# Optimization experiments

Measured on AMD Instinct MI355X. Metric: run time of the kernel, lower is better.

The kernel has to match this reference:

```python
import jax, jax.numpy as jnp
import numpy as np

B, T, C, H, L, E, K, V = 4, 1024, 1024, 16, 2, 8, 2, 32000
HD = C // H
CAP = B * T * K // E  # expert capacity with capacity_factor=1.0 -> 2048


def setup_inputs() -> dict:
    key = jax.random.key(0)
    ks = iter(jax.random.split(key, 16))
    def rn(shape, s=0.02):
        return jax.random.normal(next(ks), shape, jnp.float32) * s
    return {
        'input_ids': jax.random.randint(next(ks), (B, T), 0, V),
        'noise': jax.random.normal(next(ks), (L, B, T, E), jnp.float32),
        'tok_emb': rn((V, C)),
        'pos_emb': rn((T, C)),
        'ln1_w': jnp.ones((L, C)), 'ln1_b': jnp.zeros((L, C)),
        'qkv_w': rn((L, 3 * C, C)), 'out_w': rn((L, C, C)),
        'ln2_w': jnp.ones((L, C)), 'ln2_b': jnp.zeros((L, C)),
        'rt_w': rn((L, E, C)), 'rt_b': jnp.zeros((L, E)),
        'nz_w': rn((L, E, C)), 'nz_b': jnp.zeros((L, E)),
        'e_w1': rn((L, E, 4 * C, C)), 'e_b1': jnp.zeros((L, E, 4 * C)),
        'e_w2': rn((L, E, C, 4 * C)), 'e_b2': jnp.zeros((L, E, C)),
        'lnf_w': jnp.ones((C,)), 'lnf_b': jnp.zeros((C,)),
        'head_w': rn((1, C)), 'head_b': jnp.zeros((1,)),
    }


def _ln(x, w, b):
    m = jnp.mean(x, -1, keepdims=True)
    v = jnp.mean(jnp.square(x - m), -1, keepdims=True)
    return (x - m) * jax.lax.rsqrt(v + 1e-5) * w + b


def _attn(x, qkv_w, out_w):
    # non-causal flash-attention equivalent (softmax_scale = 1/sqrt(head_size))
    qkv = (x @ qkv_w.T).reshape(B, T, 3, H, HD)
    q, k, v = qkv[:, :, 0], qkv[:, :, 1], qkv[:, :, 2]
    s = jnp.einsum('bthd,bshd->bhts', q, k) / np.float32(np.sqrt(HD))
    p = jax.nn.softmax(s, axis=-1)
    o = jnp.einsum('bhts,bshd->bthd', p, v).reshape(B, T, C)
    return o @ out_w.T


def _moe(x, rt_w, rt_b, nz_w, nz_b, w1, b1, w2, b2, noise):
    logits = x @ rt_w.T + rt_b                      # [B,T,E]
    noise_logits = x @ nz_w.T + nz_b
    noisy = logits + noise * jax.nn.softplus(noise_logits)
    topv, topi = jax.lax.top_k(noisy, K)            # [B,T,K]
    gates = jax.nn.softmax(topv, axis=-1)           # softmax over sparse (-inf filled) logits == softmax over top-k
    oh = jax.nn.one_hot(topi, E, dtype=x.dtype)     # [B,T,K,E]
    router = jnp.einsum('btk,btke->bte', gates, oh)
    N = B * T
    flat_x = x.reshape(N, C)
    flat_r = router.reshape(N, E)
    flat_i = topi.reshape(N, K)
    updates = jnp.zeros_like(flat_x)
    for i in range(E):  # per-expert gather -> FFN -> scatter, capacity-limited in token order
        mask = jnp.any(flat_i == i, axis=-1)        # [N]
        pos = jnp.cumsum(mask) - 1
        keep = mask & (pos < CAP)
        sel = jnp.argsort(jnp.logical_not(keep))[:CAP]  # stable: kept tokens first, original order
        valid = keep[sel].astype(x.dtype)
        xi = flat_x[sel]                             # [CAP,C]
        h = jax.nn.relu(xi @ w1[i].T + b1[i])
        out = h @ w2[i].T + b2[i]
        gate = flat_r[sel, i] * valid
        updates = updates.at[sel].add(out * gate[:, None])
    return updates.reshape(B, T, C)


def reference(input_ids, noise, tok_emb, pos_emb, ln1_w, ln1_b, qkv_w, out_w,
              ln2_w, ln2_b, rt_w, rt_b, nz_w, nz_b, e_w1, e_b1, e_w2, e_b2,
              lnf_w, lnf_b, head_w, head_b):
    x = tok_emb[input_ids] + pos_emb[None, :T]
    for l in range(L):
        x = x + _attn(_ln(x, ln1_w[l], ln1_b[l]), qkv_w[l], out_w[l])
        x = x + _moe(_ln(x, ln2_w[l], ln2_b[l]), rt_w[l], rt_b[l], nz_w[l], nz_b[l],
                     e_w1[l], e_b1[l], e_w2[l], e_b2[l], noise[l])
    x = _ln(x, lnf_w, lnf_b)
    return jnp.mean(x, axis=1) @ head_w.T + head_b  # [B,1]
```

## Files before the change

kernel.cpp:

```cpp
#include <hip/hip_runtime.h>
#include <hip/hip_bf16.h>
#include <math.h>

namespace {

constexpr int B = 4, T = 1024, C = 1024, Hh = 16, L = 2, E = 8, HD = 64;
constexpr int NTOK = B * T;
constexpr int CAP = 1024;
constexpr int C3 = 3 * C, C4 = 4 * C;

typedef __attribute__((ext_vector_type(8))) short bf16x8;
typedef __attribute__((ext_vector_type(8))) short short8;
typedef __attribute__((ext_vector_type(4))) float f32x4;

static __device__ __forceinline__ short f2b(float f) {
  __hip_bfloat16 h = __float2bfloat16(f);
  return *reinterpret_cast<short*>(&h);
}
static __device__ __forceinline__ float b2f(unsigned short u) {
  union { unsigned int i; float f; } v; v.i = (unsigned int)u << 16; return v.f;
}

#define SWZ(row, kb) (((row) << 7) + ((kb) ^ (((row) & 7) << 4)))

static __device__ __forceinline__ void gload16(const void* g, void* l) {
  __builtin_amdgcn_global_load_lds((const __attribute__((address_space(1))) void*)g,
                                   (__attribute__((address_space(3))) void*)l, 16, 0, 0);
}

__global__ __launch_bounds__(256) void cvt4_kernel(
    const float* __restrict__ s0, const float* __restrict__ s1,
    const float* __restrict__ s2, const float* __restrict__ s3,
    unsigned short* __restrict__ d0, unsigned short* __restrict__ d1,
    unsigned short* __restrict__ d2, unsigned short* __restrict__ d3) {
  constexpr size_t N0 = (size_t)L * C3 * C, N1 = (size_t)L * C * C;
  constexpr size_t N2 = (size_t)L * E * C4 * C;
  size_t i = ((size_t)blockIdx.x * 256 + threadIdx.x) * 16;
  const float* s; unsigned short* d; size_t off;
  if (i < N0)                { s = s0; d = d0; off = i; }
  else if (i < N0 + N1)      { s = s1; d = d1; off = i - N0; }
  else if (i < N0 + N1 + N2) { s = s2; d = d2; off = i - N0 - N1; }
  else                       { s = s3; d = d3; off = i - N0 - N1 - N2; }
  float4 v0 = *(const float4*)(s + off);
  float4 v1 = *(const float4*)(s + off + 4);
  float4 v2 = *(const float4*)(s + off + 8);
  float4 v3 = *(const float4*)(s + off + 12);
  short8 r0, r1;
  r0[0] = f2b(v0.x); r0[1] = f2b(v0.y); r0[2] = f2b(v0.z); r0[3] = f2b(v0.w);
  r0[4] = f2b(v1.x); r0[5] = f2b(v1.y); r0[6] = f2b(v1.z); r0[7] = f2b(v1.w);
  r1[0] = f2b(v2.x); r1[1] = f2b(v2.y); r1[2] = f2b(v2.z); r1[3] = f2b(v2.w);
  r1[4] = f2b(v3.x); r1[5] = f2b(v3.y); r1[6] = f2b(v3.z); r1[7] = f2b(v3.w);
  *(short8*)(d + off) = r0;
  *(short8*)(d + off + 8) = r1;
}

__global__ __launch_bounds__(256) void embed_kernel(const int* __restrict__ ids,
    const float* __restrict__ tok, const float* __restrict__ pos, float* __restrict__ x) {
  int idx = blockIdx.x * 256 + threadIdx.x;
  int n = idx >> 8;
  int c4 = idx & 255;
  int t = n & (T - 1);
  int id = ids[n];
  float4 a = ((const float4*)(tok + (size_t)id * C))[c4];
  float4 p = ((const float4*)(pos + (size_t)t * C))[c4];
  float4 r{a.x + p.x, a.y + p.y, a.z + p.z, a.w + p.w};
  ((float4*)x)[idx] = r;
}

__global__ __launch_bounds__(256) void ln_kernel(const float* __restrict__ in,
    const unsigned short* __restrict__ eo, const int* __restrict__ slot0,
    const int* __restrict__ slot1, float* __restrict__ xupd,
    float* __restrict__ out, unsigned short* __restrict__ outb,
    const float* __restrict__ w, const float* __restrict__ b) {
  constexpr size_t SLICE = (size_t)E * CAP * C;
  __shared__ float red[8];
  int row = blockIdx.x, tid = threadIdx.x;
  float4 v = ((const float4*)(in + (size_t)row * C))[tid];
  if (eo) {
    int s0 = slot0[row], s1 = slot1[row];
    auto addslot = [&](int s) {
      if (s < 0) return;
      const unsigned short* p0 = eo + (size_t)s * C + tid * 4;
      short4 u = *(const short4*)p0;
      short4 u2 = *(const short4*)(p0 + SLICE);
      v.x += b2f((unsigned short)u.x) + b2f((unsigned short)u2.x);
      v.y += b2f((unsigned short)u.y) + b2f((unsigned short)u2.y);
      v.z += b2f((unsigned short)u.z) + b2f((unsigned short)u2.z);
      v.w += b2f((unsigned short)u.w) + b2f((unsigned short)u2.w);
    };
    addslot(s0);
    addslot(s1);
    if (xupd) ((float4*)(xupd + (size_t)row * C))[tid] = v;
  }
  float s = v.x + v.y + v.z + v.w;
  #pragma unroll
  for (int off = 32; off > 0; off >>= 1) s += __shfl_down(s, off);
  if ((tid & 63) == 0) red[tid >> 6] = s;
  __syncthreads();
  float mean = (red[0] + red[1] + red[2] + red[3]) * (1.f / C);
  __syncthreads();
  float dx = v.x - mean, dy = v.y - mean, dz = v.z - mean, dw = v.w - mean;
  float sq = dx * dx + dy * dy + dz * dz + dw * dw;
  #pragma unroll
  for (int off = 32; off > 0; off >>= 1) sq += __shfl_down(sq, off);
  if ((tid & 63) == 0) red[tid >> 6] = sq;
  __syncthreads();
  float var = (red[0] + red[1] + red[2] + red[3]) * (1.f / C);
  float rs = rsqrtf(var + 1e-5f);
  float4 wc = ((const float4*)w)[tid];
  float4 bc = ((const float4*)b)[tid];
  float4 o{dx * rs * wc.x + bc.x, dy * rs * wc.y + bc.y,
           dz * rs * wc.z + bc.z, dw * rs * wc.w + bc.w};
  if (out) ((float4*)(out + (size_t)row * C))[tid] = o;
  if (outb) {
    short4 ob{f2b(o.x), f2b(o.y), f2b(o.z), f2b(o.w)};
    *(short4*)(outb + (size_t)row * C + tid * 4) = ob;
  }
}

__global__ __launch_bounds__(256) void ln2_router_kernel(const float* __restrict__ in,
    unsigned short* __restrict__ outb,
    const float* __restrict__ w, const float* __restrict__ b,
    const float* __restrict__ rt_w, const float* __restrict__ rt_b,
    const float* __restrict__ nz_w, const float* __restrict__ nz_b,
    const float* __restrict__ noise,
    int* __restrict__ i0, int* __restrict__ i1, float* __restrict__ g0,
    float* __restrict__ g1, int* __restrict__ slot0, int* __restrict__ slot1)
{
  __shared__ float red[8];
  __shared__ float racc[4][16];
  int row = blockIdx.x, tid = threadIdx.x;
  float4 v = ((const float4*)(in + (size_t)row * C))[tid];
  float s = v.x + v.y + v.z + v.w;
  #pragma unroll
  for (int off = 32; off > 0; off >>= 1) s += __shfl_down(s, off);
  if ((tid & 63) == 0) red[tid >> 6] = s;
  __syncthreads();
  float mean = (red[0] + red[1] + red[2] + red[3]) * (1.f / C);
  __syncthreads();
  float dx = v.x - mean, dy = v.y - mean, dz = v.z - mean, dw = v.w - mean;
  float sq = dx * dx + dy * dy + dz * dz + dw * dw;
  #pragma unroll
  for (int off = 32; off > 0; off >>= 1) sq += __shfl_down(sq, off);
  if ((tid & 63) == 0) red[tid >> 6] = sq;
  __syncthreads();
  float var = (red[0] + red[1] + red[2] + red[3]) * (1.f / C);
  float rs = rsqrtf(var + 1e-5f);
  float4 wc = ((const float4*)w)[tid];
  float4 bc = ((const float4*)b)[tid];
  float4 o{dx * rs * wc.x + bc.x, dy * rs * wc.y + bc.y,
           dz * rs * wc.z + bc.z, dw * rs * wc.w + bc.w};
  short4 ob{f2b(o.x), f2b(o.y), f2b(o.z), f2b(o.w)};
  *(short4*)(outb + (size_t)row * C + tid * 4) = ob;

  float loc[16];
  #pragma unroll
  for (int e = 0; e < 8; e++) {
    float4 rw = *(const float4*)(rt_w + (size_t)e * C + tid * 4);
    float4 nw = *(const float4*)(nz_w + (size_t)e * C + tid * 4);
    loc[e]     = o.x * rw.x + o.y * rw.y + o.z * rw.z + o.w * rw.w;
    loc[8 + e] = o.x * nw.x + o.y * nw.y + o.z * nw.z + o.w * nw.w;
  }
  #pragma unroll
  for (int e = 0; e < 16; e++) {
    #pragma unroll
    for (int off = 32; off > 0; off >>= 1) loc[e] += __shfl_down(loc[e], off);
  }
  if ((tid & 63) == 0) {
    #pragma unroll
    for (int e = 0; e < 16; e++) racc[tid >> 6][e] = loc[e];
  }
  __syncthreads();
  if (tid == 0) {
    float nv[8];
    #pragma unroll
    for (int e = 0; e < 8; e++) {
      float lgt = racc[0][e] + racc[1][e] + racc[2][e] + racc[3][e] + rt_b[e];
      float nl = racc[0][8 + e] + racc[1][8 + e] + racc[2][8 + e] + racc[3][8 + e] + nz_b[e];
      float sp = fmaxf(nl, 0.f) + log1pf(expf(-fabsf(nl)));
      nv[e] = lgt + noise[(size_t)row * E + e] * sp;
    }
    float v0 = -INFINITY, v1 = -INFINITY; int b0 = -1, b1 = -1;
    #pragma unroll
    for (int e = 0; e < 8; e++) {
      float vv = nv[e];
      if (vv > v0)      { v1 = v0; b1 = b0; v0 = vv; b0 = e; }
      else if (vv > v1) { v1 = vv; b1 = e; }
    }
    float ex = expf(v1 - v0);
    float inv = 1.f / (1.f + ex);
    i0[row] = b0; i1[row] = b1;
    g0[row] = inv; g1[row] = ex * inv;
    slot0[row] = -1; slot1[row] = -1;
  }
}

template<bool GATHER, bool RELU, bool BIAS, bool XCDMAP, int OUTMODE, int SPLITK>
__global__ __launch_bounds__(512, 2) void gemm8p(
    const unsigned short* __restrict__ A, const unsigned short* __restrict__ W,
    const float* __restrict__ bias, unsigned short* __restrict__ Cout,
    const int* __restrict__ rowidx, const float* __restrict__ rowscale,
    const int* __restrict__ cnts, int M, int N, int Kd,
    size_t strideA, size_t strideW, size_t strideOut, int strideBias, int GY)
{
  __shared__ alignas(16) char smem[131072];
  int bx, by, e, ksl;
  if constexpr (XCDMAP) {
    int fid = blockIdx.x; e = fid & 7; int r1 = fid >> 3;
    ksl = r1 & (SPLITK - 1); int wi = r1 / SPLITK;
    by = wi % GY; bx = wi / GY;
  } else { bx = blockIdx.x; by = blockIdx.y; e = 0; ksl = 0; }
  int Mr = M;
  if (cnts) { int cc = cnts[e]; Mr = cc < M ? cc : M; }
  int row0 = by * 256, col0 = bx * 256;
  if (row0 >= Mr) return;

  const int kLen = Kd / SPLITK;
  const unsigned short* Ap = A + (size_t)e * strideA;
  const unsigned short* Wp = W + (size_t)e * strideW;
  const int* ridx = rowidx ? rowidx + (size_t)e * CAP : nullptr;

  int t = threadIdx.x;
  int l = t & 63, lm = l & 15, lg = l >> 4;
  int w = t >> 6, wm = w >> 2, wn = w & 3;

  const char* srcA[2];
  const char* srcB[2];
  #pragma unroll
  for (int j = 0; j < 2; j++) {
    int flat = t + j * 512;
    int row = flat >> 2;
    int c16 = (flat & 3) ^ ((row >> 1) & 3);
    int ga;
    if constexpr (GATHER) {
      int ar = row0 + row; if (ar >= Mr) ar = Mr - 1; ga = ridx[ar];
    } else ga = row0 + row;
    srcA[j] = (const char*)Ap + (size_t)ga * Kd * 2 + (size_t)ksl * kLen * 2 + c16 * 16;
    srcB[j] = (const char*)Wp + (size_t)(col0 + row) * Kd * 2 + (size_t)ksl * kLen * 2 + c16 * 16;
  }
  int dst0 = t * 16, dst1 = t * 16 + 8192;

  auto STAGE = [&](int buf, int op, int kh, int kt) {
    size_t goff = (size_t)kt * 128 + kh * 64;
    char* base = smem + buf * 65536 + op * 32768 + kh * 16384;
    if (op) {
      gload16(srcB[0] + goff, base + dst0);
      gload16(srcB[1] + goff, base + dst1);
    } else {
      gload16(srcA[0] + goff, base + dst0);
      gload16(srcA[1] + goff, base + dst1);
    }
  };

  int colswz = (lg ^ ((lm >> 1) & 3)) * 16;

  f32x4 acc[8][4];
  #pragma unroll
  for (int i = 0; i < 8; i++)
    #pragma unroll
    for (int j = 0; j < 4; j++) acc[i][j] = f32x4{0.f, 0.f, 0.f, 0.f};

  STAGE(0, 0, 0, 0); STAGE(0, 1, 0, 0); STAGE(0, 0, 1, 0); STAGE(0, 1, 1, 0);
  asm volatile("s_waitcnt vmcnt(0)" ::: "memory");
  __builtin_amdgcn_s_barrier();

  int NT = kLen >> 6;
  bf16x8 bfr[4];
  for (int k = 0; k < NT; k++) {
    int cur = k & 1, nxt = cur ^ 1;
    bool pf = (k + 1 < NT);
    #pragma unroll
    for (int ph = 0; ph < 4; ph++) {
      const int ks = ph >> 1, mh = ph & 1;
      bf16x8 afr[4];
      #pragma unroll
      for (int i = 0; i < 4; i++) {
        int row = wm * 128 + (mh * 4 + i) * 16 + lm;
        afr[i] = *(const bf16x8*)(smem + cur * 65536 + ks * 16384 + row * 64 + colswz);
      }
      if (mh == 0) {
        #pragma unroll
        for (int i = 0; i < 4; i++) {
          int row = wn * 64 + i * 16 + lm;
          bfr[i] = *(const bf16x8*)(smem + cur * 65536 + 32768 + ks * 16384 + row * 64 + colswz);
        }
      }
      if (pf) STAGE(nxt, mh, ks, k + 1);
      if (mh == 1) {
        if (pf) asm volatile("s_waitcnt vmcnt(4)" ::: "memory");
        else    asm volatile("s_waitcnt vmcnt(0)" ::: "memory");
      }
      __builtin_amdgcn_s_barrier();
      __builtin_amdgcn_s_setprio(1);
      #pragma unroll
      for (int i = 0; i < 4; i++)
        #pragma unroll
        for (int ni = 0; ni < 4; ni++)
          acc[mh * 4 + i][ni] =
              __builtin_amdgcn_mfma_f32_16x16x32_bf16(afr[i], bfr[ni], acc[mh * 4 + i][ni], 0, 0, 0);
      __builtin_amdgcn_s_setprio(0);
      __builtin_amdgcn_s_barrier();
    }
  }

  float cbias[4];
  #pragma unroll
  for (int ni = 0; ni < 4; ni++)
    cbias[ni] = (BIAS && ksl == 0) ? bias[(size_t)e * strideBias + col0 + wn * 64 + ni * 16 + lm] : 0.f;

  #pragma unroll
  for (int mi = 0; mi < 8; mi++) {
    #pragma unroll
    for (int rr = 0; rr < 4; rr++) {
      int m = row0 + wm * 128 + mi * 16 + lg * 4 + rr;
      if (m >= Mr) continue;
      if constexpr (OUTMODE == 0) {
        unsigned short* cp = Cout + (size_t)e * strideOut + (size_t)m * N + col0 + wn * 64 + lm;
        #pragma unroll
        for (int ni = 0; ni < 4; ni++) {
          float v = acc[mi][ni][rr] + cbias[ni];
          if constexpr (RELU) v = fmaxf(v, 0.f);
          cp[ni * 16] = (unsigned short)f2b(v);
        }
      } else {
        float sc = rowscale[(size_t)e * CAP + m];
        unsigned short* cp = Cout + (size_t)ksl * ((size_t)E * CAP * N)
                             + ((size_t)e * CAP + m) * N + col0 + wn * 64 + lm;
        #pragma unroll
        for (int ni = 0; ni < 4; ni++) {
          float v = acc[mi][ni][rr] + cbias[ni];
          cp[ni * 16] = (unsigned short)f2b(sc * v);
        }
      }
    }
  }
}

__global__ __launch_bounds__(256) void gemm_proj(
    const unsigned short* __restrict__ A, const unsigned short* __restrict__ W,
    float* __restrict__ Cout, int M, int N, int Kd)
{
  int bx = blockIdx.x, by = blockIdx.y;
  int row0 = by * 128, col0 = bx * 128;

  __shared__ alignas(16) char smem[32768];
  char* Ab = smem;
  char* Bb = smem + 16384;

  int t = threadIdx.x, w = t >> 6, l = t & 63;
  int lm = l & 15, lg = l >> 4;
  int wr = w >> 1, wc = w & 1;

  int lrow8 = l >> 3;
  int scol = ((l & 7) ^ lrow8) << 4;
  const char* srcA[4];
  const char* srcB[4];
  #pragma unroll
  for (int i = 0; i < 4; i++) {
    int seg = w * 4 + i;
    int rloc = seg * 8 + lrow8;
    srcA[i] = (const char*)A + (size_t)(row0 + rloc) * Kd * 2 + scol;
    srcB[i] = (const char*)W + (size_t)(col0 + rloc) * Kd * 2 + scol;
  }

  f32x4 acc[4][4];
  #pragma unroll
  for (int i = 0; i < 4; i++)
    #pragma unroll
    for (int j = 0; j < 4; j++) acc[i][j] = f32x4{0.f, 0.f, 0.f, 0.f};

  int NT = Kd >> 6;
  for (int kt = 0; kt < NT; kt++) {
    __syncthreads();
    #pragma unroll
    for (int i = 0; i < 4; i++) {
      int seg = w * 4 + i;
      gload16(srcA[i], Ab + seg * 1024);
      gload16(srcB[i], Bb + seg * 1024);
      srcA[i] += 128;
      srcB[i] += 128;
    }
    __syncthreads();
    #pragma unroll
    for (int ks = 0; ks < 2; ks++) {
      bf16x8 af[4], bfr[4];
      #pragma unroll
      for (int mi = 0; mi < 4; mi++)
        af[mi] = *(const bf16x8*)(Ab + SWZ(wr * 64 + mi * 16 + lm, ks * 64 + lg * 16));
      #pragma unroll
      for (int ni = 0; ni < 4; ni++)
        bfr[ni] = *(const bf16x8*)(Bb + SWZ(wc * 64 + ni * 16 + lm, ks * 64 + lg * 16));
      #pragma unroll
      for (int mi = 0; mi < 4; mi++)
        #pragma unroll
        for (int ni = 0; ni < 4; ni++)
          acc[mi][ni] = __builtin_amdgcn_mfma_f32_16x16x32_bf16(af[mi], bfr[ni], acc[mi][ni], 0, 0, 0);
    }
  }

  #pragma unroll
  for (int mi = 0; mi < 4; mi++) {
    #pragma unroll
    for (int rr = 0; rr < 4; rr++) {
      int m = row0 + wr * 64 + mi * 16 + lg * 4 + rr;
      float* cp = Cout + (size_t)m * N + col0 + wc * 64 + lm;
      #pragma unroll
      for (int ni = 0; ni < 4; ni++) cp[ni * 16] += acc[mi][ni][rr];
    }
  }
}

__global__ __launch_bounds__(256) void attn_mfma(const unsigned short* __restrict__ qkv,
                                                 unsigned short* __restrict__ ao) {
  __shared__ alignas(16) char smem[20480];
  char* Ks = smem;
  char* Vt = smem + 4096;
  char* Pb = smem + 12288;

  int t = threadIdx.x, w = t >> 6, lane = t & 63, lm = lane & 15, lg = lane >> 4;
  int qt = blockIdx.x, bh = blockIdx.y, b = bh >> 4, h = bh & 15;
  const unsigned short* base = qkv + (size_t)b * T * C3;

  bf16x8 qf[2];
  {
    int qrow = qt * 64 + w * 16 + lm;
    const unsigned short* qp = base + (size_t)qrow * C3 + h * HD + lg * 8;
    qf[0] = *(const bf16x8*)qp;
    qf[1] = *(const bf16x8*)(qp + 32);
  }

  f32x4 o[4];
  #pragma unroll
  for (int i = 0; i < 4; i++) o[i] = f32x4{0.f, 0.f, 0.f, 0.f};
  float mrun[4] = {-INFINITY, -INFINITY, -INFINITY, -INFINITY};
  float lpart[4] = {0.f, 0.f, 0.f, 0.f};

  int ksrow = t >> 3, kc = (t & 7) * 8;
  int vdl = t & 7;
  bf16x8 kreg;
  unsigned short vv[8];
  auto LOADKV = [&](int s0) {
    kreg = *(const bf16x8*)(base + (size_t)(s0 + ksrow) * C3 + C + h * HD + kc);
    const unsigned short* vp = base + (size_t)(s0 + ksrow) * C3 + 2 * C + h * HD + vdl;
    #pragma unroll
    for (int i = 0; i < 8; i++) vv[i] = vp[8 * i];
  };

  LOADKV(0);
  for (int s0 = 0; s0 < T; s0 += 32) {
    __syncthreads();
    *(bf16x8*)(Ks + SWZ(ksrow, kc * 2)) = kreg;
    #pragma unroll
    for (int i = 0; i < 8; i++) {
      int d = 8 * i + vdl;
      *(short*)(Vt + (d << 7) + ((ksrow * 2) ^ ((d & 7) << 4))) = (short)vv[i];
    }
    __syncthreads();
    if (s0 + 32 < T) LOADKV(s0 + 32);

    f32x4 sacc[2];
    sacc[0] = f32x4{0.f, 0.f, 0.f, 0.f};
    sacc[1] = f32x4{0.f, 0.f, 0.f, 0.f};
    #pragma unroll
    for (int ni = 0; ni < 2; ni++)
      #pragma unroll
      for (int ks = 0; ks < 2; ks++) {
        bf16x8 kfrag = *(const bf16x8*)(Ks + SWZ(ni * 16 + lm, ks * 64 + lg * 16));
        sacc[ni] = __builtin_amdgcn_mfma_f32_16x16x32_bf16(qf[ks], kfrag, sacc[ni], 0, 0, 0);
      }

    float sv0[4], sv1[4], pv[8];
    bool okd = true;
    #pragma unroll
    for (int r = 0; r < 4; r++) {
      sv0[r] = sacc[0][r] * 0.125f;
      sv1[r] = sacc[1][r] * 0.125f;
      okd = okd && (fmaxf(sv0[r], sv1[r]) <= mrun[r] + 8.f);
    }
    if (__all(okd ? 1 : 0)) {
      #pragma unroll
      for (int r = 0; r < 4; r++) {
        float p0 = __expf(sv0[r] - mrun[r]);
        float p1 = __expf(sv1[r] - mrun[r]);
        lpart[r] += p0 + p1;
        pv[r] = p0; pv[4 + r] = p1;
      }
    } else {
      float fr[4];
      #pragma unroll
      for (int r = 0; r < 4; r++) {
        float tmax = fmaxf(sv0[r], sv1[r]);
        #pragma unroll
        for (int mk = 1; mk < 16; mk <<= 1) tmax = fmaxf(tmax, __shfl_xor(tmax, mk));
        float mn = fmaxf(mrun[r], tmax);
        float f = __expf(mrun[r] - mn);
        float p0 = __expf(sv0[r] - mn), p1 = __expf(sv1[r] - mn);
        lpart[r] = lpart[r] * f + p0 + p1;
        mrun[r] = mn;
        fr[r] = f;
        pv[r] = p0; pv[4 + r] = p1;
      }
      #pragma unroll
      for (int ni = 0; ni < 4; ni++) {
        o[ni][0] *= fr[0]; o[ni][1] *= fr[1]; o[ni][2] *= fr[2]; o[ni][3] *= fr[3];
      }
    }

    char* P = Pb + w * 2048;
    #pragma unroll
    for (int ni = 0; ni < 2; ni++)
      #pragma unroll
      for (int r = 0; r < 4; r++) {
        int q = lg * 4 + r;
        int kbyte = (ni * 16 + lm) * 2;
        *(short*)(P + (q << 7) + (kbyte ^ ((q & 7) << 4))) = f2b(pv[ni * 4 + r]);
      }
    bf16x8 pfrag = *(const bf16x8*)(P + SWZ(lm, lg * 16));
    #pragma unroll
    for (int ni = 0; ni < 4; ni++) {
      bf16x8 vfrag = *(const bf16x8*)(Vt + SWZ(ni * 16 + lm, lg * 16));
      o[ni] = __builtin_amdgcn_mfma_f32_16x16x32_bf16(pfrag, vfrag, o[ni], 0, 0, 0);
    }
  }

  float inv[4];
  #pragma unroll
  for (int r = 0; r < 4; r++) {
    float lsum = lpart[r];
    #pragma unroll
    for (int mk = 1; mk < 16; mk <<= 1) lsum += __shfl_xor(lsum, mk);
    inv[r] = 1.f / lsum;
  }
  #pragma unroll
  for (int r = 0; r < 4; r++) {
    int qrow = qt * 64 + w * 16 + lg * 4 + r;
    unsigned short* dst = ao + (size_t)(b * T + qrow) * C + h * HD + lm;
    #pragma unroll
    for (int ni = 0; ni < 4; ni++) dst[ni * 16] = (unsigned short)f2b(o[ni][r] * inv[r]);
  }
}

__global__ __launch_bounds__(512) void capacity_kernel(
    const int* __restrict__ i0, const int* __restrict__ i1,
    const float* __restrict__ g0, const float* __restrict__ g1,
    int* __restrict__ sel, float* __restrict__ gsel, int* __restrict__ counts,
    int* __restrict__ slot0, int* __restrict__ slot1)
{
  int e = threadIdx.x >> 6, lane = threadIdx.x & 63;
  int cnt = 0;
  unsigned long long ltmask = (lane == 0) ? 0ull : (~0ull >> (64 - lane));
  int a = i0[lane], bb = i1[lane];
  for (int basei = 0; basei < NTOK; basei += 64) {
    int na = 0, nb = 0;
    if (basei + 64 < NTOK) { na = i0[basei + 64 + lane]; nb = i1[basei + 64 + lane]; }
    int tt = basei + lane;
    bool match = (a == e) || (bb == e);
    unsigned long long mk = __ballot(match);
    int pos = cnt + __popcll(mk & ltmask);
    if (match && pos < CAP) {
      sel[e * CAP + pos] = tt;
      gsel[e * CAP + pos] = (a == e) ? g0[tt] : g1[tt];
      if (a == e) slot0[tt] = e * CAP + pos;
      else        slot1[tt] = e * CAP + pos;
    }
    cnt += __popcll(mk);
    a = na; bb = nb;
  }
  if (lane == 0) counts[e] = cnt < CAP ? cnt : CAP;
}

__global__ __launch_bounds__(256) void head_part(const float* __restrict__ xin,
    const float* __restrict__ hw, float* __restrict__ partial)
{
  __shared__ float red[8];
  int blk = blockIdx.x;
  int b = blk >> 4, j = blk & 15;
  int tid = threadIdx.x;
  float4 wv = ((const float4*)hw)[tid];
  float s = 0.f;
  int t0 = j * 64;
  for (int t = t0; t < t0 + 64; t++) {
    float4 v = ((const float4*)(xin + (size_t)(b * T + t) * C))[tid];
    s += v.x * wv.x + v.y * wv.y + v.z * wv.z + v.w * wv.w;
  }
  #pragma unroll
  for (int off = 32; off > 0; off >>= 1) s += __shfl_down(s, off);
  if ((tid & 63) == 0) red[tid >> 6] = s;
  __syncthreads();
  if (tid == 0) partial[blk] = red[0] + red[1] + red[2] + red[3];
}

__global__ __launch_bounds__(64) void head_final(const float* __restrict__ partial,
    const float* __restrict__ hb, float* __restrict__ out)
{
  int tid = threadIdx.x;
  float v = partial[tid];
  #pragma unroll
  for (int off = 8; off > 0; off >>= 1) v += __shfl_down(v, off, 16);
  if ((tid & 15) == 0) out[tid >> 4] = v * (1.f / T) + hb[0];
}

}

extern "C" void kernel_launch(void* const* d_in, const int* in_sizes, int n_in,
                              void* d_out, int out_size, void* d_ws, size_t ws_size,
                              hipStream_t stream) {
  (void)in_sizes; (void)n_in; (void)out_size; (void)ws_size;
  const int*   ids     = (const int*)d_in[0];
  const float* noise   = (const float*)d_in[1];
  const float* tok_emb = (const float*)d_in[2];
  const float* pos_emb = (const float*)d_in[3];
  const float* ln1_w   = (const float*)d_in[4];
  const float* ln1_b   = (const float*)d_in[5];
  const float* qkv_w   = (const float*)d_in[6];
  const float* out_w   = (const float*)d_in[7];
  const float* ln2_w   = (const float*)d_in[8];
  const float* ln2_b   = (const float*)d_in[9];
  const float* rt_w    = (const float*)d_in[10];
  const float* rt_b    = (const float*)d_in[11];
  const float* nz_w    = (const float*)d_in[12];
  const float* nz_b    = (const float*)d_in[13];
  const float* e_w1    = (const float*)d_in[14];
  const float* e_b1    = (const float*)d_in[15];
  const float* e_w2    = (const float*)d_in[16];
  const float* e_b2    = (const float*)d_in[17];
  const float* lnf_w   = (const float*)d_in[18];
  const float* lnf_b   = (const float*)d_in[19];
  const float* head_w  = (const float*)d_in[20];
  const float* head_b  = (const float*)d_in[21];
  float* out = (float*)d_out;

  char* wsp = (char*)d_ws;
  size_t off = 0;
  auto alloc = [&](size_t n) { char* p = wsp + off; off += (n + 255) & ~(size_t)255; return p; };
  float* x    = (float*)alloc((size_t)NTOK * C * 4);
  float* t1   = (float*)alloc((size_t)NTOK * C * 4);
  unsigned short* t1b  = (unsigned short*)alloc((size_t)NTOK * C * 2);
  unsigned short* qkvb = (unsigned short*)alloc((size_t)NTOK * C3 * 2);
  unsigned short* aob  = (unsigned short*)alloc((size_t)NTOK * C * 2);
  unsigned short* hbuf = (unsigned short*)alloc((size_t)E * CAP * C4 * 2);
  unsigned short* eo   = (unsigned short*)alloc((size_t)2 * E * CAP * C * 2);
  unsigned short* qkvw_b = (unsigned short*)alloc((size_t)L * C3 * C * 2);
  unsigned short* outw_b = (unsigned short*)alloc((size_t)L * C * C * 2);
  unsigned short* ew1_b  = (unsigned short*)alloc((size_t)L * E * C4 * C * 2);
  unsigned short* ew2_b  = (unsigned short*)alloc((size_t)L * E * C * C4 * 2);
  int*   i0   = (int*)alloc(NTOK * 4);
  int*   i1   = (int*)alloc(NTOK * 4);
  float* g0   = (float*)alloc(NTOK * 4);
  float* g1   = (float*)alloc(NTOK * 4);
  int*   sel  = (int*)alloc(E * CAP * 4);
  float* gsel = (float*)alloc(E * CAP * 4);
  int*   counts = (int*)alloc(E * 4);
  int*   slot0  = (int*)alloc(NTOK * 4);
  int*   slot1  = (int*)alloc(NTOK * 4);
  float* hpart  = (float*)alloc(B * 16 * 4);

  {
    constexpr size_t TOT = (size_t)L * C3 * C + (size_t)L * C * C + 2 * (size_t)L * E * C4 * C;
    cvt4_kernel<<<(int)(TOT / 4096), 256, 0, stream>>>(qkv_w, out_w, e_w1, e_w2,
                                                       qkvw_b, outw_b, ew1_b, ew2_b);
  }

  embed_kernel<<<NTOK * C / 4 / 256, 256, 0, stream>>>(ids, tok_emb, pos_emb, x);

  for (int l = 0; l < L; l++) {
    if (l == 0)
      ln_kernel<<<NTOK, 256, 0, stream>>>(x, nullptr, nullptr, nullptr, nullptr,
                                          nullptr, t1b, ln1_w + l * C, ln1_b + l * C);
    else
      ln_kernel<<<NTOK, 256, 0, stream>>>(x, eo, slot0, slot1, x,
                                          nullptr, t1b, ln1_w + l * C, ln1_b + l * C);
    gemm8p<false, false, false, false, 0, 1><<<dim3(C3 / 256, NTOK / 256), 512, 0, stream>>>(
        t1b, qkvw_b + (size_t)l * C3 * C, nullptr, qkvb,
        nullptr, nullptr, nullptr, NTOK, C3, C, 0, 0, 0, 0, 0);
    attn_mfma<<<dim3(T / 64, B * Hh), 256, 0, stream>>>(qkvb, aob);
    gemm_proj<<<dim3(C / 128, NTOK / 128), 256, 0, stream>>>(
        aob, outw_b + (size_t)l * C * C, x, NTOK, C, C);

    ln2_router_kernel<<<NTOK, 256, 0, stream>>>(x, t1b, ln2_w + l * C, ln2_b + l * C,
        rt_w + (size_t)l * E * C, rt_b + l * E, nz_w + (size_t)l * E * C, nz_b + l * E,
        noise + (size_t)l * NTOK * E, i0, i1, g0, g1, slot0, slot1);
    capacity_kernel<<<1, 512, 0, stream>>>(i0, i1, g0, g1, sel, gsel, counts, slot0, slot1);

    gemm8p<true, true, true, true, 0, 1><<<(C4 / 256) * (CAP / 256) * E, 512, 0, stream>>>(
        t1b, ew1_b + (size_t)l * E * C4 * C, e_b1 + (size_t)l * E * C4, hbuf,
        sel, nullptr, counts, CAP, C4, C,
        0, (size_t)C4 * C, (size_t)CAP * C4, C4, CAP / 256);
    gemm8p<false, false, true, true, 2, 2><<<(C / 256) * (CAP / 256) * 2 * E, 512, 0, stream>>>(
        hbuf, ew2_b + (size_t)l * E * C * C4, e_b2 + (size_t)l * E * C, eo,
        nullptr, gsel, counts, CAP, C, C4,
        (size_t)CAP * C4, (size_t)C * C4, 0, C, CAP / 256);
  }

  ln_kernel<<<NTOK, 256, 0, stream>>>(x, eo, slot0, slot1, nullptr,
                                      t1, nullptr, lnf_w, lnf_b);
  head_part<<<B * 16, 256, 0, stream>>>(t1, head_w, hpart);
  head_final<<<1, 64, 0, stream>>>(hpart, head_b, out);
}
```

Baseline: 838.8 us.

## Fuse fp32-to-bf16 weight conversion into GEMM B-operand loading

Drops the standalone pass that converted the qkv and expert weights to bf16. The GEMM now reads fp32 weights straight into registers, packs them to bf16 and writes them into swizzled LDS, with a reworked double-buffer schedule and manual waitcnt management. This removes a large read and write pass over the expert weights. In exchange it doubles weight bytes read inside the GEMM, where they are read by several row tiles, and adds register pressure and VALU conversion work in the main loop.

```diff
diff --git a/kernel.cpp b/kernel.cpp
--- a/kernel.cpp
+++ b/kernel.cpp
@@ -20,6 +20,12 @@
 static __device__ __forceinline__ float b2f(unsigned short u) {
   union { unsigned int i; float f; } v; v.i = (unsigned int)u << 16; return v.f;
 }
+static __device__ __forceinline__ bf16x8 pack8(float4 a, float4 b) {
+  bf16x8 r;
+  r[0] = f2b(a.x); r[1] = f2b(a.y); r[2] = f2b(a.z); r[3] = f2b(a.w);
+  r[4] = f2b(b.x); r[5] = f2b(b.y); r[6] = f2b(b.z); r[7] = f2b(b.w);
+  return r;
+}
 
 #define SWZ(row, kb) (((row) << 7) + ((kb) ^ (((row) & 7) << 4)))
 
@@ -28,30 +34,15 @@
                                    (__attribute__((address_space(3))) void*)l, 16, 0, 0);
 }
 
-__global__ __launch_bounds__(256) void cvt4_kernel(
-    const float* __restrict__ s0, const float* __restrict__ s1,
-    const float* __restrict__ s2, const float* __restrict__ s3,
-    unsigned short* __restrict__ d0, unsigned short* __restrict__ d1,
-    unsigned short* __restrict__ d2, unsigned short* __restrict__ d3) {
-  constexpr size_t N0 = (size_t)L * C3 * C, N1 = (size_t)L * C * C;
-  constexpr size_t N2 = (size_t)L * E * C4 * C;
-  size_t i = ((size_t)blockIdx.x * 256 + threadIdx.x) * 16;
-  const float* s; unsigned short* d; size_t off;
-  if (i < N0)                { s = s0; d = d0; off = i; }
-  else if (i < N0 + N1)      { s = s1; d = d1; off = i - N0; }
-  else if (i < N0 + N1 + N2) { s = s2; d = d2; off = i - N0 - N1; }
-  else                       { s = s3; d = d3; off = i - N0 - N1 - N2; }
-  float4 v0 = *(const float4*)(s + off);
-  float4 v1 = *(const float4*)(s + off + 4);
-  float4 v2 = *(const float4*)(s + off + 8);
-  float4 v3 = *(const float4*)(s + off + 12);
-  short8 r0, r1;
-  r0[0] = f2b(v0.x); r0[1] = f2b(v0.y); r0[2] = f2b(v0.z); r0[3] = f2b(v0.w);
-  r0[4] = f2b(v1.x); r0[5] = f2b(v1.y); r0[6] = f2b(v1.z); r0[7] = f2b(v1.w);
-  r1[0] = f2b(v2.x); r1[1] = f2b(v2.y); r1[2] = f2b(v2.z); r1[3] = f2b(v2.w);
-  r1[4] = f2b(v3.x); r1[5] = f2b(v3.y); r1[6] = f2b(v3.z); r1[7] = f2b(v3.w);
-  *(short8*)(d + off) = r0;
-  *(short8*)(d + off + 8) = r1;
+__global__ __launch_bounds__(256) void cvt_kernel(const float* __restrict__ in,
+    unsigned short* __restrict__ out) {
+  size_t i = ((size_t)blockIdx.x * 256 + threadIdx.x) * 8;
+  float4 v0 = *(const float4*)(in + i);
+  float4 v1 = *(const float4*)(in + i + 4);
+  short8 r;
+  r[0] = f2b(v0.x); r[1] = f2b(v0.y); r[2] = f2b(v0.z); r[3] = f2b(v0.w);
+  r[4] = f2b(v1.x); r[5] = f2b(v1.y); r[6] = f2b(v1.z); r[7] = f2b(v1.w);
+  *(short8*)(out + i) = r;
 }
 
 __global__ __launch_bounds__(256) void embed_kernel(const int* __restrict__ ids,
@@ -197,7 +188,7 @@
 
 template<bool GATHER, bool RELU, bool BIAS, bool XCDMAP, int OUTMODE, int SPLITK>
 __global__ __launch_bounds__(512, 2) void gemm8p(
-    const unsigned short* __restrict__ A, const unsigned short* __restrict__ W,
+    const unsigned short* __restrict__ A, const float* __restrict__ W,
     const float* __restrict__ bias, unsigned short* __restrict__ Cout,
     const int* __restrict__ rowidx, const float* __restrict__ rowscale,
     const int* __restrict__ cnts, int M, int N, int Kd,
@@ -217,7 +208,7 @@
 
   const int kLen = Kd / SPLITK;
   const unsigned short* Ap = A + (size_t)e * strideA;
-  const unsigned short* Wp = W + (size_t)e * strideW;
+  const float* Wp = W + (size_t)e * strideW;
   const int* ridx = rowidx ? rowidx + (size_t)e * CAP : nullptr;
 
   int t = threadIdx.x;
@@ -225,7 +216,6 @@
   int w = t >> 6, wm = w >> 2, wn = w & 3;
 
   const char* srcA[2];
-  const char* srcB[2];
   #pragma unroll
   for (int j = 0; j < 2; j++) {
     int flat = t + j * 512;
@@ -236,22 +226,42 @@
       int ar = row0 + row; if (ar >= Mr) ar = Mr - 1; ga = ridx[ar];
     } else ga = row0 + row;
     srcA[j] = (const char*)Ap + (size_t)ga * Kd * 2 + (size_t)ksl * kLen * 2 + c16 * 16;
-    srcB[j] = (const char*)Wp + (size_t)(col0 + row) * Kd * 2 + (size_t)ksl * kLen * 2 + c16 * 16;
   }
   int dst0 = t * 16, dst1 = t * 16 + 8192;
-
-  auto STAGE = [&](int buf, int op, int kh, int kt) {
-    size_t goff = (size_t)kt * 128 + kh * 64;
-    char* base = smem + buf * 65536 + op * 32768 + kh * 16384;
-    if (op) {
-      gload16(srcB[0] + goff, base + dst0);
-      gload16(srcB[1] + goff, base + dst1);
-    } else {
-      gload16(srcA[0] + goff, base + dst0);
-      gload16(srcA[1] + goff, base + dst1);
-    }
+  auto STAGEA = [&](int buf, int kt) {
+    size_t g = (size_t)kt * 128;
+    char* base = smem + buf * 65536;
+    gload16(srcA[0] + g, base + dst0);
+    gload16(srcA[1] + g, base + dst1);
+    gload16(srcA[0] + g + 64, base + 16384 + dst0);
+    gload16(srcA[1] + g + 64, base + 16384 + dst1);
   };
 
+  int brow = t & 255;
+  int bc16 = (t >> 8) * 2;
+  const float* bsrc = Wp + (size_t)(col0 + brow) * Kd + (size_t)ksl * kLen;
+  float4 bregA[8], bregB[8];
+  auto LOADB = [&](float4* br, int kt) {
+    const float* p = bsrc + kt * 64;
+    #pragma unroll
+    for (int kh = 0; kh < 2; kh++)
+      #pragma unroll
+      for (int j = 0; j < 2; j++) {
+        br[kh * 4 + j * 2]     = *(const float4*)(p + kh * 32 + (bc16 + j) * 8);
+        br[kh * 4 + j * 2 + 1] = *(const float4*)(p + kh * 32 + (bc16 + j) * 8 + 4);
+      }
+  };
+  auto WRITEB = [&](float4* br, int buf) {
+    #pragma unroll
+    for (int kh = 0; kh < 2; kh++)
+      #pragma unroll
+      for (int j = 0; j < 2; j++) {
+        int c16s = (bc16 + j) ^ ((brow >> 1) & 3);
+        *(bf16x8*)(smem + buf * 65536 + 32768 + kh * 16384 + brow * 64 + c16s * 16)
+            = pack8(br[kh * 4 + j * 2], br[kh * 4 + j * 2 + 1]);
+      }
+  };
+
   int colswz = (lg ^ ((lm >> 1) & 3)) * 16;
 
   f32x4 acc[8][4];
@@ -260,15 +270,18 @@
     #pragma unroll
     for (int j = 0; j < 4; j++) acc[i][j] = f32x4{0.f, 0.f, 0.f, 0.f};
 
-  STAGE(0, 0, 0, 0); STAGE(0, 1, 0, 0); STAGE(0, 0, 1, 0); STAGE(0, 1, 1, 0);
-  asm volatile("s_waitcnt vmcnt(0)" ::: "memory");
+  int NT = kLen >> 6;
+
+  LOADB(bregA, 0);
+  STAGEA(0, 0);
+  LOADB(bregB, 1);
+  WRITEB(bregA, 0);
+  asm volatile("s_waitcnt vmcnt(8)" ::: "memory");
+  asm volatile("s_waitcnt lgkmcnt(0)" ::: "memory");
   __builtin_amdgcn_s_barrier();
 
-  int NT = kLen >> 6;
   bf16x8 bfr[4];
-  for (int k = 0; k < NT; k++) {
-    int cur = k & 1, nxt = cur ^ 1;
-    bool pf = (k + 1 < NT);
+  auto PHASES = [&](int cbase, int obase, auto stage_fn, auto write_fn) {
     #pragma unroll
     for (int ph = 0; ph < 4; ph++) {
       const int ks = ph >> 1, mh = ph & 1;
@@ -276,20 +289,17 @@
       #pragma unroll
       for (int i = 0; i < 4; i++) {
         int row = wm * 128 + (mh * 4 + i) * 16 + lm;
-        afr[i] = *(const bf16x8*)(smem + cur * 65536 + ks * 16384 + row * 64 + colswz);
+        afr[i] = *(const bf16x8*)(smem + cbase + ks * 16384 + row * 64 + colswz);
       }
       if (mh == 0) {
         #pragma unroll
         for (int i = 0; i < 4; i++) {
           int row = wn * 64 + i * 16 + lm;
-          bfr[i] = *(const bf16x8*)(smem + cur * 65536 + 32768 + ks * 16384 + row * 64 + colswz);
+          bfr[i] = *(const bf16x8*)(smem + cbase + 32768 + ks * 16384 + row * 64 + colswz);
         }
       }
-      if (pf) STAGE(nxt, mh, ks, k + 1);
-      if (mh == 1) {
-        if (pf) asm volatile("s_waitcnt vmcnt(4)" ::: "memory");
-        else    asm volatile("s_waitcnt vmcnt(0)" ::: "memory");
-      }
+      stage_fn(ph);
+      if (ph == 3) write_fn();
       __builtin_amdgcn_s_barrier();
       __builtin_amdgcn_s_setprio(1);
       #pragma unroll
@@ -301,6 +311,36 @@
       __builtin_amdgcn_s_setprio(0);
       __builtin_amdgcn_s_barrier();
     }
+    (void)obase;
+  };
+
+  for (int k = 0; k < NT; k += 2) {
+    bool pfW2 = (k + 2 < NT);
+    bool pfW3 = (k + 3 < NT);
+    PHASES(0, 65536,
+      [&](int ph) {
+        if (ph == 0) STAGEA(1, k + 1);
+        if (ph == 1 && pfW2) LOADB(bregA, k + 2);
+      },
+      [&]() {
+        WRITEB(bregB, 1);
+        if (pfW2) asm volatile("s_waitcnt vmcnt(8)" ::: "memory");
+        else      asm volatile("s_waitcnt vmcnt(0)" ::: "memory");
+        asm volatile("s_waitcnt lgkmcnt(0)" ::: "memory");
+      });
+    PHASES(65536, 0,
+      [&](int ph) {
+        if (ph == 0 && pfW2) STAGEA(0, k + 2);
+        if (ph == 1 && pfW3) LOADB(bregB, k + 3);
+      },
+      [&]() {
+        if (pfW2) {
+          WRITEB(bregA, 0);
+          if (pfW3) asm volatile("s_waitcnt vmcnt(8)" ::: "memory");
+          else      asm volatile("s_waitcnt vmcnt(0)" ::: "memory");
+          asm volatile("s_waitcnt lgkmcnt(0)" ::: "memory");
+        }
+      });
   }
 
   float cbias[4];
@@ -640,10 +680,7 @@
   unsigned short* aob  = (unsigned short*)alloc((size_t)NTOK * C * 2);
   unsigned short* hbuf = (unsigned short*)alloc((size_t)E * CAP * C4 * 2);
   unsigned short* eo   = (unsigned short*)alloc((size_t)2 * E * CAP * C * 2);
-  unsigned short* qkvw_b = (unsigned short*)alloc((size_t)L * C3 * C * 2);
   unsigned short* outw_b = (unsigned short*)alloc((size_t)L * C * C * 2);
-  unsigned short* ew1_b  = (unsigned short*)alloc((size_t)L * E * C4 * C * 2);
-  unsigned short* ew2_b  = (unsigned short*)alloc((size_t)L * E * C * C4 * 2);
   int*   i0   = (int*)alloc(NTOK * 4);
   int*   i1   = (int*)alloc(NTOK * 4);
   float* g0   = (float*)alloc(NTOK * 4);
@@ -655,11 +692,7 @@
   int*   slot1  = (int*)alloc(NTOK * 4);
   float* hpart  = (float*)alloc(B * 16 * 4);
 
-  {
-    constexpr size_t TOT = (size_t)L * C3 * C + (size_t)L * C * C + 2 * (size_t)L * E * C4 * C;
-    cvt4_kernel<<<(int)(TOT / 4096), 256, 0, stream>>>(qkv_w, out_w, e_w1, e_w2,
-                                                       qkvw_b, outw_b, ew1_b, ew2_b);
-  }
+  cvt_kernel<<<(int)((size_t)L * C * C / 2048), 256, 0, stream>>>(out_w, outw_b);
 
   embed_kernel<<<NTOK * C / 4 / 256, 256, 0, stream>>>(ids, tok_emb, pos_emb, x);
 
@@ -671,7 +704,7 @@
       ln_kernel<<<NTOK, 256, 0, stream>>>(x, eo, slot0, slot1, x,
                                           nullptr, t1b, ln1_w + l * C, ln1_b + l * C);
     gemm8p<false, false, false, false, 0, 1><<<dim3(C3 / 256, NTOK / 256), 512, 0, stream>>>(
-        t1b, qkvw_b + (size_t)l * C3 * C, nullptr, qkvb,
+        t1b, qkv_w + (size_t)l * C3 * C, nullptr, qkvb,
         nullptr, nullptr, nullptr, NTOK, C3, C, 0, 0, 0, 0, 0);
     attn_mfma<<<dim3(T / 64, B * Hh), 256, 0, stream>>>(qkvb, aob);
     gemm_proj<<<dim3(C / 128, NTOK / 128), 256, 0, stream>>>(
@@ -683,11 +716,11 @@
     capacity_kernel<<<1, 512, 0, stream>>>(i0, i1, g0, g1, sel, gsel, counts, slot0, slot1);
 
     gemm8p<true, true, true, true, 0, 1><<<(C4 / 256) * (CAP / 256) * E, 512, 0, stream>>>(
-        t1b, ew1_b + (size_t)l * E * C4 * C, e_b1 + (size_t)l * E * C4, hbuf,
+        t1b, e_w1 + (size_t)l * E * C4 * C, e_b1 + (size_t)l * E * C4, hbuf,
         sel, nullptr, counts, CAP, C4, C,
         0, (size_t)C4 * C, (size_t)CAP * C4, C4, CAP / 256);
     gemm8p<false, false, true, true, 2, 2><<<(C / 256) * (CAP / 256) * 2 * E, 512, 0, stream>>>(
-        hbuf, ew2_b + (size_t)l * E * C * C4, e_b2 + (size_t)l * E * C, eo,
+        hbuf, e_w2 + (size_t)l * E * C * C4, e_b2 + (size_t)l * E * C, eo,
         nullptr, gsel, counts, CAP, C, C4,
         (size_t)CAP * C4, (size_t)C * C4, 0, C, CAP / 256);
   }
```

After: 1.705 ms. +103.2%, slower.
